# Kernel optimization log

Measured on AMD Instinct MI355X. Metric: run time of the kernel, lower is better.

## Reference

```python
import jax, jax.numpy as jnp
import numpy as np

N, E, F, H, O, R = 50000, 600000, 128, 128, 64, 8


def setup_inputs() -> dict:
    key = jax.random.key(0)
    ks = jax.random.split(key, 10)
    x = jax.random.normal(ks[0], (N, F), dtype=jnp.float32)
    edge_index = jax.random.randint(ks[1], (2, E), 0, N, dtype=jnp.int64)
    edge_weight = jax.random.uniform(ks[2], (E,), dtype=jnp.float32)
    edge_type = jax.random.randint(ks[3], (E,), 0, R, dtype=jnp.int64)
    s = 1.0 / np.sqrt(F)
    W1 = jax.random.uniform(ks[4], (R, F, H), jnp.float32, -s, s)
    root1 = jax.random.uniform(ks[5], (F, H), jnp.float32, -s, s)
    bias1 = jnp.zeros((H,), jnp.float32)
    sh = 1.0 / np.sqrt(H)
    W2 = jax.random.uniform(ks[6], (R, H, O), jnp.float32, -sh, sh)
    root2 = jax.random.uniform(ks[7], (H, O), jnp.float32, -sh, sh)
    bias2 = jnp.zeros((O,), jnp.float32)
    return {"x": x, "edge_index": edge_index, "edge_weight": edge_weight,
            "edge_type": edge_type, "W1": W1, "root1": root1, "bias1": bias1,
            "W2": W2, "root2": root2, "bias2": bias2}


def _rgcn_conv(x, src, dst, et, ew, W, root, bias, num_nodes):
    # project every node by every relation: [N, R, out] (cheaper than per-edge
    # materialization of weight[edge_type] which is E x in x out)
    proj = jnp.einsum('nd,rdo->nro', x, W)
    # per-edge message = x_j @ W[edge_type] * edge_weight  -> [E, out]
    msg = proj[src, et] * ew[:, None]
    # weighted scatter-mean over destination nodes
    agg = jax.ops.segment_sum(msg, dst, num_segments=num_nodes)
    cnt = jax.ops.segment_sum(jnp.ones_like(ew), dst, num_segments=num_nodes)
    agg = agg / jnp.maximum(cnt, 1.0)[:, None]
    # root (self) transform + bias
    return agg + x @ root + bias


def reference(x, edge_index, edge_weight, edge_type, W1, root1, bias1, W2, root2, bias2):
    src, dst = edge_index[0], edge_index[1]
    et = edge_type.astype(jnp.int32)
    # min-max normalize edge weights as in RGCN.forward
    ew = (edge_weight - edge_weight.min()) / (edge_weight.max() - edge_weight.min() + 1e-8)
    n = x.shape[0]
    h = jax.nn.relu(_rgcn_conv(x, src, dst, et, ew, W1, root1, bias1, n))
    return _rgcn_conv(h, src, dst, et, ew, W2, root2, bias2, n)
```

## Files before the change

kernel.cpp:

```cpp
#include <hip/hip_runtime.h>

#define F_DIM 128
#define H_DIM 128
#define O_DIM 64
#define R_NUM 8

typedef __attribute__((ext_vector_type(8))) short bf16x8;
typedef __attribute__((ext_vector_type(4))) float f32x4;
typedef __attribute__((ext_vector_type(8))) unsigned short u16x8;

union V8 { bf16x8 v; short4 h[2]; };

__device__ __forceinline__ unsigned short f2b(float f) {
    unsigned u = __float_as_uint(f);
    u += 0x7FFFu + ((u >> 16) & 1u);
    return (unsigned short)(u >> 16);
}
__device__ __forceinline__ float b2f(unsigned short b) {
    return __uint_as_float(((unsigned)b) << 16);
}

__global__ void count_minmax(const float* __restrict__ ew, const int* __restrict__ dst,
                             const int* __restrict__ et, int* __restrict__ deg2,
                             float* __restrict__ bmn, float* __restrict__ bmx, int E) {
    __shared__ float smn[256], smx[256];
    int tid = threadIdx.x;
    float mn = 1e30f, mx = -1e30f;
    for (int i = blockIdx.x * blockDim.x + tid; i < E; i += gridDim.x * blockDim.x) {
        atomicAdd(&deg2[dst[i] * R_NUM + et[i]], 1);
        float v = ew[i];
        mn = fminf(mn, v);
        mx = fmaxf(mx, v);
    }
    smn[tid] = mn; smx[tid] = mx;
    __syncthreads();
    for (int s = 128; s > 0; s >>= 1) {
        if (tid < s) {
            smn[tid] = fminf(smn[tid], smn[tid + s]);
            smx[tid] = fmaxf(smx[tid], smx[tid + s]);
        }
        __syncthreads();
    }
    if (tid == 0) { bmn[blockIdx.x] = smn[0]; bmx[blockIdx.x] = smx[0]; }
}

__global__ void convert_bf16(const float* __restrict__ in, unsigned short* __restrict__ out,
                             long n4) {
    long i = (long)blockIdx.x * blockDim.x + threadIdx.x;
    if (i >= n4) return;
    float4 v = ((const float4*)in)[i];
    ushort4 o;
    o.x = f2b(v.x); o.y = f2b(v.y); o.z = f2b(v.z); o.w = f2b(v.w);
    ((ushort4*)out)[i] = o;
}

__global__ void conv_weights(const float* __restrict__ W1, const float* __restrict__ root1,
                             const float* __restrict__ W2, const float* __restrict__ root2,
                             unsigned short* __restrict__ wt1,
                             unsigned short* __restrict__ wt2) {
    const int n1 = 9 * 128 * 128, n2 = 9 * 64 * 128;
    int idx = blockIdx.x * blockDim.x + threadIdx.x;
    if (idx < n1) {
        int r = idx / (128 * 128), rem = idx % (128 * 128);
        int n = rem / 128, k = rem % 128;
        float v = (r < 8) ? W1[((size_t)r * 128 + k) * 128 + n] : root1[(size_t)k * 128 + n];
        wt1[idx] = f2b(v);
    } else if (idx < n1 + n2) {
        int j = idx - n1;
        int r = j / (64 * 128), rem = j % (64 * 128);
        int n = rem / 128, k = rem % 128;
        float v = (r < 8) ? W2[((size_t)r * 128 + k) * 64 + n] : root2[(size_t)k * 64 + n];
        wt2[j] = f2b(v);
    }
}

__global__ void scan1_kernel(const int* __restrict__ deg, int* __restrict__ rp,
                             int* __restrict__ bsum, float* __restrict__ invc,
                             int M, int N) {
    __shared__ int s[256];
    int base = blockIdx.x * 2048;
    int t = threadIdx.x;
    int v[8]; int loc = 0;
#pragma unroll
    for (int i = 0; i < 8; ++i) {
        int idx = base + t * 8 + i;
        v[i] = (idx < M) ? deg[idx] : 0;
        loc += v[i];
    }
    int node = blockIdx.x * 256 + t;
    if (node < N) invc[node] = 1.0f / (float)max(loc, 1);
    s[t] = loc;
    __syncthreads();
    for (int off = 1; off < 256; off <<= 1) {
        int x = (t >= off) ? s[t - off] : 0;
        __syncthreads();
        s[t] += x;
        __syncthreads();
    }
    int run = s[t] - loc;
#pragma unroll
    for (int i = 0; i < 8; ++i) {
        int idx = base + t * 8 + i;
        if (idx < M) rp[idx] = run;
        run += v[i];
    }
    if (t == 255) bsum[blockIdx.x] = s[255];
}

__global__ void scan2_mm(int* bsum, int nb, const float* __restrict__ bmn,
                         const float* __restrict__ bmx, float* mm) {
    __shared__ int s[256];
    __shared__ float smn[256], smx[256];
    int t = threadIdx.x;
    int v = (t < nb) ? bsum[t] : 0;
    s[t] = v;
    float mn = fminf(bmn[t], bmn[t + 256]);
    float mx = fmaxf(bmx[t], bmx[t + 256]);
    smn[t] = mn; smx[t] = mx;
    __syncthreads();
    for (int off = 1; off < 256; off <<= 1) {
        int x = (t >= off) ? s[t - off] : 0;
        __syncthreads();
        s[t] += x;
        __syncthreads();
    }
    if (t < nb) bsum[t] = s[t] - v;
    for (int r = 128; r > 0; r >>= 1) {
        if (t < r) {
            smn[t] = fminf(smn[t], smn[t + r]);
            smx[t] = fmaxf(smx[t], smx[t + r]);
        }
        __syncthreads();
    }
    if (t == 0) { mm[0] = smn[0]; mm[1] = smx[0]; }
}

__global__ void scan3_kernel(int* __restrict__ rp, const int* __restrict__ bsum, int M) {
    int i = blockIdx.x * blockDim.x + threadIdx.x;
    if (i < M) rp[i] += bsum[i >> 11];
}

__global__ void fill2_kernel(const int* __restrict__ src, const int* __restrict__ dst,
                             const int* __restrict__ et, const float* __restrict__ ew,
                             const float* __restrict__ mm, int* __restrict__ rp2,
                             int2* __restrict__ erec, int E) {
    int e = blockIdx.x * blockDim.x + threadIdx.x;
    if (e >= E) return;
    int pos = atomicAdd(&rp2[dst[e] * R_NUM + et[e]], 1);
    float mn = mm[0], mx = mm[1];
    erec[pos] = make_int2(src[e], __float_as_int((ew[e] - mn) / (mx - mn + 1e-8f)));
}

__global__ __launch_bounds__(256) void gather_y(
    const int* __restrict__ rp2, const int2* __restrict__ erec,
    const unsigned short* __restrict__ inp, const float* __restrict__ invc,
    unsigned short* __restrict__ y, int N) {
    int gid = blockIdx.x * blockDim.x + threadIdx.x;
    int grp = gid >> 4;
    int n = grp >> 3;
    if (n >= N) return;
    int r = grp & 7;
    int j = (gid & 15) * 8;
    int i = n * R_NUM + r;
    int beg = (i == 0) ? 0 : rp2[i - 1];
    int end = rp2[i];
    float acc[8] = {0.f, 0.f, 0.f, 0.f, 0.f, 0.f, 0.f, 0.f};
    for (int k = beg; k < end; ++k) {
        int2 e = erec[k];
        float w = __int_as_float(e.y);
        const u16x8 v = *(const u16x8*)(inp + (size_t)e.x * 128 + j);
#pragma unroll
        for (int c = 0; c < 8; ++c) acc[c] += w * b2f(v[c]);
    }
    float inv = invc[n];
    u16x8 o;
#pragma unroll
    for (int c = 0; c < 8; ++c) o[c] = f2b(acc[c] * inv);
    *(u16x8*)(y + ((size_t)n * R_NUM + r) * 128 + j) = o;
}

template <int NCOL, bool RELU, bool OUTB>
__global__ __launch_bounds__(256) void gemm_y(
    const unsigned short* __restrict__ y,
    const unsigned short* __restrict__ inp,
    const unsigned short* __restrict__ Wt,
    const float* __restrict__ bias,
    unsigned short* __restrict__ outb, float* __restrict__ outf, int N)
{
    constexpr int NT = NCOL / 16;
    __shared__ unsigned short smem[64 * 132 + NCOL * 132];
    unsigned short* ys  = smem;
    unsigned short* wsd = smem + 64 * 132;

    const int tid = threadIdx.x;
    const int w = tid >> 6, lane = tid & 63;
    const int quad = lane >> 4, l15 = lane & 15;
    const int n0 = blockIdx.x * 64;

    f32x4 acc[NT];
#pragma unroll
    for (int nt = 0; nt < NT; ++nt) acc[nt] = (f32x4){0.f, 0.f, 0.f, 0.f};

    for (int r = 0; r < 9; ++r) {
#pragma unroll
        for (int it = 0; it < NCOL / 16; ++it) {
            int u = tid + it * 256;
            int row = u >> 4, seg = u & 15;
            V8 v;
            v.v = *(const bf16x8*)(Wt + ((size_t)r * NCOL + row) * 128 + seg * 8);
            *(short4*)&wsd[row * 132 + seg * 8]     = v.h[0];
            *(short4*)&wsd[row * 132 + seg * 8 + 4] = v.h[1];
        }
#pragma unroll
        for (int it = 0; it < 4; ++it) {
            int u = tid + it * 256;
            int row = u >> 4, seg = u & 15;
            int node = n0 + row;
            if (node >= N) node = N - 1;
            const unsigned short* src = (r < 8)
                ? y + ((size_t)node * R_NUM + r) * 128 + seg * 8
                : inp + (size_t)node * 128 + seg * 8;
            V8 v; v.v = *(const bf16x8*)src;
            *(short4*)&ys[row * 132 + seg * 8]     = v.h[0];
            *(short4*)&ys[row * 132 + seg * 8 + 4] = v.h[1];
        }
        __syncthreads();
        const unsigned short* yrow = ys + (size_t)(w * 16 + l15) * 132 + quad * 8;
#pragma unroll
        for (int k2 = 0; k2 < 4; ++k2) {
            V8 b;
            b.h[0] = *(const short4*)(yrow + k2 * 32);
            b.h[1] = *(const short4*)(yrow + k2 * 32 + 4);
#pragma unroll
            for (int nt = 0; nt < NT; ++nt) {
                const unsigned short* ar = wsd + (size_t)(nt * 16 + l15) * 132
                                           + k2 * 32 + quad * 8;
                V8 av;
                av.h[0] = *(const short4*)ar;
                av.h[1] = *(const short4*)(ar + 4);
                acc[nt] = __builtin_amdgcn_mfma_f32_16x16x32_bf16(av.v, b.v, acc[nt], 0, 0, 0);
            }
        }
        __syncthreads();
    }

    const int gn = tid >> 2, gq = tid & 3;
    const int gnode = n0 + gn;
    if (OUTB) {
        unsigned short* stg = smem;
#pragma unroll
        for (int nt = 0; nt < NT; ++nt) {
            int c0 = nt * 16 + quad * 4;
            float4 bs = *(const float4*)(bias + c0);
            float v0 = acc[nt][0] + bs.x, v1 = acc[nt][1] + bs.y;
            float v2 = acc[nt][2] + bs.z, v3 = acc[nt][3] + bs.w;
            if (RELU) {
                v0 = fmaxf(v0, 0.f); v1 = fmaxf(v1, 0.f);
                v2 = fmaxf(v2, 0.f); v3 = fmaxf(v3, 0.f);
            }
            short4 o;
            o.x = (short)f2b(v0); o.y = (short)f2b(v1);
            o.z = (short)f2b(v2); o.w = (short)f2b(v3);
            *(short4*)&stg[(w * 16 + l15) * 136 + c0] = o;
        }
        __syncthreads();
        if (gnode < N) {
            const unsigned short* srow = stg + gn * 136 + gq * (NCOL / 4);
            unsigned short* drow = outb + (size_t)gnode * NCOL + gq * (NCOL / 4);
#pragma unroll
            for (int c = 0; c < NCOL / 32; ++c)
                *(bf16x8*)(drow + c * 8) = *(const bf16x8*)(srow + c * 8);
        }
    } else {
        float* stg = (float*)smem;
#pragma unroll
        for (int nt = 0; nt < NT; ++nt) {
            int c0 = nt * 16 + quad * 4;
            float4 bs = *(const float4*)(bias + c0);
            float v0 = acc[nt][0] + bs.x, v1 = acc[nt][1] + bs.y;
            float v2 = acc[nt][2] + bs.z, v3 = acc[nt][3] + bs.w;
            if (RELU) {
                v0 = fmaxf(v0, 0.f); v1 = fmaxf(v1, 0.f);
                v2 = fmaxf(v2, 0.f); v3 = fmaxf(v3, 0.f);
            }
            *(float4*)&stg[(w * 16 + l15) * 68 + c0] = make_float4(v0, v1, v2, v3);
        }
        __syncthreads();
        if (gnode < N) {
            const float* srow = stg + gn * 68 + gq * (NCOL / 4);
            float* drow = outf + (size_t)gnode * NCOL + gq * (NCOL / 4);
#pragma unroll
            for (int c = 0; c < NCOL / 16; ++c)
                *(float4*)(drow + c * 4) = *(const float4*)(srow + c * 4);
        }
    }
}

extern "C" void kernel_launch(void* const* d_in, const int* in_sizes, int n_in,
                              void* d_out, int out_size, void* d_ws, size_t ws_size,
                              hipStream_t stream) {
    const float* x     = (const float*)d_in[0];
    const int*   ei    = (const int*)d_in[1];
    const float* ew    = (const float*)d_in[2];
    const int*   et    = (const int*)d_in[3];
    const float* W1    = (const float*)d_in[4];
    const float* root1 = (const float*)d_in[5];
    const float* bias1 = (const float*)d_in[6];
    const float* W2    = (const float*)d_in[7];
    const float* root2 = (const float*)d_in[8];
    const float* bias2 = (const float*)d_in[9];

    const int N = in_sizes[0] / F_DIM;
    const int E = in_sizes[2];
    const int M2 = N * R_NUM;
    const int* srcp = ei;
    const int* dstp = ei + E;

    int* base = (int*)d_ws;
    float* mm    = (float*)base;
    float* invc  = (float*)(base + 16);
    int*   deg2  = base + 16 + N;
    int*   rp2   = deg2 + M2;
    int*   bsum  = rp2 + M2;
    float* bmn   = (float*)(bsum + 256);
    float* bmx   = bmn + 512;
    int2*  erec  = (int2*)(bmx + 512);
    unsigned short* xb  = (unsigned short*)((int*)erec + 2 * E);
    unsigned short* hb  = xb + (size_t)N * 128;
    unsigned short* wt1 = hb + (size_t)N * 128;
    unsigned short* wt2 = wt1 + 9 * 128 * 128;
    unsigned short* y   = wt2 + 9 * 64 * 128;

    const int TB = 256;
    int blocksE = (E + TB - 1) / TB;
    int nb = (M2 + 2047) / 2048;

    hipMemsetAsync(deg2, 0, (size_t)M2 * sizeof(int), stream);
    count_minmax<<<512, TB, 0, stream>>>(ew, dstp, et, deg2, bmn, bmx, E);
    long x4 = (long)N * 128 / 4;
    convert_bf16<<<(int)((x4 + TB - 1) / TB), TB, 0, stream>>>(x, xb, x4);
    int wtot = 9 * 128 * 128 + 9 * 64 * 128;
    conv_weights<<<(wtot + TB - 1) / TB, TB, 0, stream>>>(W1, root1, W2, root2, wt1, wt2);
    scan1_kernel<<<nb, TB, 0, stream>>>(deg2, rp2, bsum, invc, M2, N);
    scan2_mm<<<1, TB, 0, stream>>>(bsum, nb, bmn, bmx, mm);
    scan3_kernel<<<(M2 + TB - 1) / TB, TB, 0, stream>>>(rp2, bsum, M2);
    fill2_kernel<<<blocksE, TB, 0, stream>>>(srcp, dstp, et, ew, mm, rp2, erec, E);

    int gatB = (int)(((long)N * R_NUM * 16 + TB - 1) / TB);
    int gB = (N + 63) / 64;

    gather_y<<<gatB, TB, 0, stream>>>(rp2, erec, xb, invc, y, N);
    gemm_y<H_DIM, true, true><<<gB, TB, 0, stream>>>(y, xb, wt1, bias1, hb, nullptr, N);
    gather_y<<<gatB, TB, 0, stream>>>(rp2, erec, hb, invc, y, N);
    gemm_y<O_DIM, false, false><<<gB, TB, 0, stream>>>(y, hb, wt2, bias2, nullptr,
                                                       (float*)d_out, N);
}
```

Baseline: 337.5 us.

## Fuse setup kernels, pack edge records into 32 bits, widen gather parallelism

Merges the degree/minmax, x conversion and weight conversion kernels into one grid-stride kernel, cutting two launches. Edge records are packed into a single 32-bit word holding a 17-bit source index and a 15-bit truncated bf16 weight, which halves record traffic. The gather now uses 32 threads per segment, each loading 4 bf16 instead of 8, which doubles thread count. Risks: the weight loses precision (bf16 with its low mantissa bit dropped), and the 17-bit index only holds for N up to 131072.

```diff
diff --git a/kernel.cpp b/kernel.cpp
--- a/kernel.cpp
+++ b/kernel.cpp
@@ -7,7 +7,6 @@
 
 typedef __attribute__((ext_vector_type(8))) short bf16x8;
 typedef __attribute__((ext_vector_type(4))) float f32x4;
-typedef __attribute__((ext_vector_type(8))) unsigned short u16x8;
 
 union V8 { bf16x8 v; short4 h[2]; };
 
@@ -20,13 +19,21 @@
     return __uint_as_float(((unsigned)b) << 16);
 }
 
-__global__ void count_minmax(const float* __restrict__ ew, const int* __restrict__ dst,
-                             const int* __restrict__ et, int* __restrict__ deg2,
-                             float* __restrict__ bmn, float* __restrict__ bmx, int E) {
+__global__ __launch_bounds__(256) void setupA(
+    const float* __restrict__ ew, const int* __restrict__ dst,
+    const int* __restrict__ et, int E, int* __restrict__ deg2,
+    float* __restrict__ bmn, float* __restrict__ bmx,
+    const float* __restrict__ x, unsigned short* __restrict__ xb, long x4,
+    const float* __restrict__ W1, const float* __restrict__ root1,
+    const float* __restrict__ W2, const float* __restrict__ root2,
+    unsigned short* __restrict__ wt1, unsigned short* __restrict__ wt2) {
     __shared__ float smn[256], smx[256];
-    int tid = threadIdx.x;
+    const int tid = threadIdx.x;
+    const int gstride = gridDim.x * blockDim.x;
+    int g0 = blockIdx.x * blockDim.x + tid;
+
     float mn = 1e30f, mx = -1e30f;
-    for (int i = blockIdx.x * blockDim.x + tid; i < E; i += gridDim.x * blockDim.x) {
+    for (int i = g0; i < E; i += gstride) {
         atomicAdd(&deg2[dst[i] * R_NUM + et[i]], 1);
         float v = ew[i];
         mn = fminf(mn, v);
@@ -42,35 +49,30 @@
         __syncthreads();
     }
     if (tid == 0) { bmn[blockIdx.x] = smn[0]; bmx[blockIdx.x] = smx[0]; }
-}
-
-__global__ void convert_bf16(const float* __restrict__ in, unsigned short* __restrict__ out,
-                             long n4) {
-    long i = (long)blockIdx.x * blockDim.x + threadIdx.x;
-    if (i >= n4) return;
-    float4 v = ((const float4*)in)[i];
-    ushort4 o;
-    o.x = f2b(v.x); o.y = f2b(v.y); o.z = f2b(v.z); o.w = f2b(v.w);
-    ((ushort4*)out)[i] = o;
-}
-
-__global__ void conv_weights(const float* __restrict__ W1, const float* __restrict__ root1,
-                             const float* __restrict__ W2, const float* __restrict__ root2,
-                             unsigned short* __restrict__ wt1,
-                             unsigned short* __restrict__ wt2) {
+
+    for (long i = g0; i < x4; i += gstride) {
+        float4 v = ((const float4*)x)[i];
+        ushort4 o;
+        o.x = f2b(v.x); o.y = f2b(v.y); o.z = f2b(v.z); o.w = f2b(v.w);
+        ((ushort4*)xb)[i] = o;
+    }
+
     const int n1 = 9 * 128 * 128, n2 = 9 * 64 * 128;
-    int idx = blockIdx.x * blockDim.x + threadIdx.x;
-    if (idx < n1) {
-        int r = idx / (128 * 128), rem = idx % (128 * 128);
-        int n = rem / 128, k = rem % 128;
-        float v = (r < 8) ? W1[((size_t)r * 128 + k) * 128 + n] : root1[(size_t)k * 128 + n];
-        wt1[idx] = f2b(v);
-    } else if (idx < n1 + n2) {
-        int j = idx - n1;
-        int r = j / (64 * 128), rem = j % (64 * 128);
-        int n = rem / 128, k = rem % 128;
-        float v = (r < 8) ? W2[((size_t)r * 128 + k) * 64 + n] : root2[(size_t)k * 64 + n];
-        wt2[j] = f2b(v);
+    for (int idx = g0; idx < n1 + n2; idx += gstride) {
+        if (idx < n1) {
+            int r = idx / (128 * 128), rem = idx % (128 * 128);
+            int n = rem / 128, k = rem % 128;
+            float v = (r < 8) ? W1[((size_t)r * 128 + k) * 128 + n]
+                              : root1[(size_t)k * 128 + n];
+            wt1[idx] = f2b(v);
+        } else {
+            int j = idx - n1;
+            int r = j / (64 * 128), rem = j % (64 * 128);
+            int n = rem / 128, k = rem % 128;
+            float v = (r < 8) ? W2[((size_t)r * 128 + k) * 64 + n]
+                              : root2[(size_t)k * 64 + n];
+            wt2[j] = f2b(v);
+        }
     }
 }
 
@@ -114,9 +116,8 @@
     int t = threadIdx.x;
     int v = (t < nb) ? bsum[t] : 0;
     s[t] = v;
-    float mn = fminf(bmn[t], bmn[t + 256]);
-    float mx = fmaxf(bmx[t], bmx[t + 256]);
-    smn[t] = mn; smx[t] = mx;
+    smn[t] = fminf(bmn[t], bmn[t + 256]);
+    smx[t] = fmaxf(bmx[t], bmx[t + 256]);
     __syncthreads();
     for (int off = 1; off < 256; off <<= 1) {
         int x = (t >= off) ? s[t - off] : 0;
@@ -143,40 +144,39 @@
 __global__ void fill2_kernel(const int* __restrict__ src, const int* __restrict__ dst,
                              const int* __restrict__ et, const float* __restrict__ ew,
                              const float* __restrict__ mm, int* __restrict__ rp2,
-                             int2* __restrict__ erec, int E) {
+                             unsigned* __restrict__ erec, int E) {
     int e = blockIdx.x * blockDim.x + threadIdx.x;
     if (e >= E) return;
     int pos = atomicAdd(&rp2[dst[e] * R_NUM + et[e]], 1);
     float mn = mm[0], mx = mm[1];
-    erec[pos] = make_int2(src[e], __float_as_int((ew[e] - mn) / (mx - mn + 1e-8f)));
+    unsigned wq = f2b((ew[e] - mn) / (mx - mn + 1e-8f));
+    erec[pos] = (wq << 17) | (unsigned)src[e];
 }
 
 __global__ __launch_bounds__(256) void gather_y(
-    const int* __restrict__ rp2, const int2* __restrict__ erec,
+    const int* __restrict__ rp2, const unsigned* __restrict__ erec,
     const unsigned short* __restrict__ inp, const float* __restrict__ invc,
     unsigned short* __restrict__ y, int N) {
-    int gid = blockIdx.x * blockDim.x + threadIdx.x;
-    int grp = gid >> 4;
-    int n = grp >> 3;
+    int gid = blockIdx.x * 256 + threadIdx.x;
+    int seg = gid >> 5;
+    int n = seg >> 3;
     if (n >= N) return;
-    int r = grp & 7;
-    int j = (gid & 15) * 8;
-    int i = n * R_NUM + r;
-    int beg = (i == 0) ? 0 : rp2[i - 1];
-    int end = rp2[i];
-    float acc[8] = {0.f, 0.f, 0.f, 0.f, 0.f, 0.f, 0.f, 0.f};
+    int j = (gid & 31) * 4;
+    int beg = (seg == 0) ? 0 : rp2[seg - 1];
+    int end = rp2[seg];
+    float a0 = 0.f, a1 = 0.f, a2 = 0.f, a3 = 0.f;
     for (int k = beg; k < end; ++k) {
-        int2 e = erec[k];
-        float w = __int_as_float(e.y);
-        const u16x8 v = *(const u16x8*)(inp + (size_t)e.x * 128 + j);
-#pragma unroll
-        for (int c = 0; c < 8; ++c) acc[c] += w * b2f(v[c]);
+        unsigned rec = erec[k];
+        float w = __uint_as_float((rec >> 1) & 0x7FFF8000u);
+        ushort4 v = *(const ushort4*)(inp + (size_t)(rec & 0x1FFFFu) * 128 + j);
+        a0 += w * b2f(v.x); a1 += w * b2f(v.y);
+        a2 += w * b2f(v.z); a3 += w * b2f(v.w);
     }
     float inv = invc[n];
-    u16x8 o;
-#pragma unroll
-    for (int c = 0; c < 8; ++c) o[c] = f2b(acc[c] * inv);
-    *(u16x8*)(y + ((size_t)n * R_NUM + r) * 128 + j) = o;
+    ushort4 o;
+    o.x = f2b(a0 * inv); o.y = f2b(a1 * inv);
+    o.z = f2b(a2 * inv); o.w = f2b(a3 * inv);
+    *(ushort4*)(y + (size_t)seg * 128 + j) = o;
 }
 
 template <int NCOL, bool RELU, bool OUTB>
@@ -324,8 +324,8 @@
     int*   bsum  = rp2 + M2;
     float* bmn   = (float*)(bsum + 256);
     float* bmx   = bmn + 512;
-    int2*  erec  = (int2*)(bmx + 512);
-    unsigned short* xb  = (unsigned short*)((int*)erec + 2 * E);
+    unsigned* erec = (unsigned*)(bmx + 512);
+    unsigned short* xb  = (unsigned short*)(erec + E);
     unsigned short* hb  = xb + (size_t)N * 128;
     unsigned short* wt1 = hb + (size_t)N * 128;
     unsigned short* wt2 = wt1 + 9 * 128 * 128;
@@ -334,19 +334,17 @@
     const int TB = 256;
     int blocksE = (E + TB - 1) / TB;
     int nb = (M2 + 2047) / 2048;
+    long x4 = (long)N * 128 / 4;
 
     hipMemsetAsync(deg2, 0, (size_t)M2 * sizeof(int), stream);
-    count_minmax<<<512, TB, 0, stream>>>(ew, dstp, et, deg2, bmn, bmx, E);
-    long x4 = (long)N * 128 / 4;
-    convert_bf16<<<(int)((x4 + TB - 1) / TB), TB, 0, stream>>>(x, xb, x4);
-    int wtot = 9 * 128 * 128 + 9 * 64 * 128;
-    conv_weights<<<(wtot + TB - 1) / TB, TB, 0, stream>>>(W1, root1, W2, root2, wt1, wt2);
+    setupA<<<512, TB, 0, stream>>>(ew, dstp, et, E, deg2, bmn, bmx,
+                                   x, xb, x4, W1, root1, W2, root2, wt1, wt2);
     scan1_kernel<<<nb, TB, 0, stream>>>(deg2, rp2, bsum, invc, M2, N);
     scan2_mm<<<1, TB, 0, stream>>>(bsum, nb, bmn, bmx, mm);
     scan3_kernel<<<(M2 + TB - 1) / TB, TB, 0, stream>>>(rp2, bsum, M2);
     fill2_kernel<<<blocksE, TB, 0, stream>>>(srcp, dstp, et, ew, mm, rp2, erec, E);
 
-    int gatB = (int)(((long)N * R_NUM * 16 + TB - 1) / TB);
+    int gatB = (int)(((long)M2 * 32 + TB - 1) / TB);
     int gB = (N + 63) / 64;
 
     gather_y<<<gatB, TB, 0, stream>>>(rp2, erec, xb, invc, y, N);
```

Result: slower. 387.2 us (+14.7%).
